# Performance work log

Hardware: AMD Instinct MI355X
Metric: run time of the kernel (lower is better)

Reference implementation:

```python
import jax, jax.numpy as jnp
import numpy as np

B, N, C, K = 32, 1024, 14, 9      # graphs, residues/graph, atom channels, kNN
E, H, NC = 128, 128, 25           # embed_size, hidden_size, num_classes
NG = 128                          # gaussians in time embedding (== embed_size)


def _ffn(x, W1, b1, W2, b2):
    # nn.Sequential(SiLU, Linear, SiLU, Linear)
    h = jax.nn.silu(x) @ W1 + b1
    return jax.nn.silu(h) @ W2 + b2


def _time_emb(t, Wt1, bt1, Wt2, bt2):
    # GaussianSmearing(0,1,NG) -> Linear -> ReLU -> Linear
    offset = jnp.linspace(0.0, 1.0, NG)
    coeff = -0.5 / (offset[1] - offset[0]) ** 2
    d = t[..., None] - offset + 1e-6
    g = jnp.exp(coeff * d * d)
    return jax.nn.relu(g @ Wt1 + bt1) @ Wt2 + bt2


def _forward(S, X, t, emb, Wt1, bt1, Wt2, bt2, We1, be1, We2, be2,
             Wx1, bx1, Wx2, bx2, Wh1, bh1, Wh2, bh2,
             Wd1, bd1, Wd2, bd2, Wp1, bp1, Wr1, br1, Wr2, br2):
    H0 = emb[S]                                           # [B,N,E]
    Hh = H0 + _time_emb(t, Wt1, bt1, Wt2, bt2)            # H_0 + time_emb
    # dynamic kNN graph on CA coordinates (channel 1), per graph
    ca = X[:, :, 1]                                       # [B,N,3]
    d2 = jnp.sum((ca[:, :, None] - ca[:, None]) ** 2, -1) # [B,N,N]
    d2 = d2 + jnp.eye(N, dtype=d2.dtype) * 1e10           # no self loops
    _, idx = jax.lax.top_k(-d2, K)                        # [B,N,K] neighbor ids
    gather = jax.vmap(lambda a, i: a[i])                  # per-graph gather
    Xnb = gather(X, idx)                                  # [B,N,K,C,3]
    Hnb = gather(Hh, idx)                                 # [B,N,K,E]
    rel = X[:, :, None] - Xnb                             # [B,N,K,C,3]
    # multi-channel radial features (EGNN-style channel Gram matrix)
    radial = jnp.einsum('bnkcd,bnked->bnkce', rel, rel).reshape(B, N, K, C * C) / C
    Hi = jnp.broadcast_to(Hh[:, :, None], (B, N, K, E))
    m = _ffn(jnp.concatenate([Hi, Hnb, radial], -1), We1, be1, We2, be2)  # [B,N,K,H]
    # EGNN coordinate update
    w = _ffn(m, Wx1, bx1, Wx2, bx2)                       # [B,N,K,1]
    X_out = X + jnp.mean(rel * w[..., None], axis=2)      # [B,N,C,3]
    # node update
    Hn = Hh + _ffn(jnp.concatenate([Hh, jnp.sum(m, 2)], -1), Wh1, bh1, Wh2, bh2)
    # symmetric edge-distance FFN: f([src,dst]) + f([dst,src])
    Hs = jnp.broadcast_to(Hn[:, :, None], (B, N, K, E))
    Hd = gather(Hn, idx)
    pd = (_ffn(jnp.concatenate([Hs, Hd], -1), Wd1, bd1, Wd2, bd2)
          + _ffn(jnp.concatenate([Hd, Hs], -1), Wd1, bd1, Wd2, bd2))[..., 0]  # [B,N,K]
    # pred_logits = ffn_residue2(pre_H_0 * sigmoid(ffn_proj(H)))
    gate = jax.nn.sigmoid(jax.nn.silu(Hn) @ Wp1 + bp1)
    logits = _ffn(H0 * gate, Wr1, br1, Wr2, br2)          # [B,N,NC]
    return logits, X_out, pd


def setup_inputs() -> dict:
    key = jax.random.key(0)
    ks = jax.random.split(key, 34)
    p = lambda k, s: (0.02 * jax.random.normal(k, s)).astype(jnp.float32)
    inp = {
        'X': jax.random.normal(ks[0], (B, N, C, 3), jnp.float32),
        'S': jax.random.randint(ks[1], (B, N), 0, NC),
        't': jax.random.uniform(ks[2], (B, N), jnp.float32),
        'emb': p(ks[3], (NC, E)),
        'Wt1': p(ks[4], (NG, H)), 'bt1': jnp.zeros((H,), jnp.float32),
        'Wt2': p(ks[5], (H, E)), 'bt2': jnp.zeros((E,), jnp.float32),
        'We1': p(ks[6], (2 * E + C * C, H)), 'be1': jnp.zeros((H,), jnp.float32),
        'We2': p(ks[7], (H, H)), 'be2': jnp.zeros((H,), jnp.float32),
        'Wx1': p(ks[8], (H, H)), 'bx1': jnp.zeros((H,), jnp.float32),
        'Wx2': p(ks[9], (H, 1)), 'bx2': jnp.zeros((1,), jnp.float32),
        'Wh1': p(ks[10], (E + H, H)), 'bh1': jnp.zeros((H,), jnp.float32),
        'Wh2': p(ks[11], (H, E)), 'bh2': jnp.zeros((E,), jnp.float32),
        'Wd1': p(ks[12], (2 * E, H)), 'bd1': jnp.zeros((H,), jnp.float32),
        'Wd2': p(ks[13], (H, 1)), 'bd2': jnp.zeros((1,), jnp.float32),
        'Wp1': p(ks[14], (E, E)), 'bp1': jnp.zeros((E,), jnp.float32),
        'Wr1': p(ks[15], (E, H)), 'br1': jnp.zeros((H,), jnp.float32),
        'Wr2': p(ks[16], (H, NC)), 'br2': jnp.zeros((NC,), jnp.float32),
    }
    return inp


def reference(X, S, t, emb, Wt1, bt1, Wt2, bt2, We1, be1, We2, be2,
              Wx1, bx1, Wx2, bx2, Wh1, bh1, Wh2, bh2,
              Wd1, bd1, Wd2, bd2, Wp1, bp1, Wr1, br1, Wr2, br2):
    return _forward(S, X, t, emb, Wt1, bt1, Wt2, bt2, We1, be1, We2, be2,
                    Wx1, bx1, Wx2, bx2, Wh1, bh1, Wh2, bh2,
                    Wd1, bd1, Wd2, bd2, Wp1, bp1, Wr1, br1, Wr2, br2)
```

## Files before the change

kernel.cpp:

```cpp
#include <hip/hip_runtime.h>

#define BATCH 32
#define NPT   1024
#define CC    14
#define KNN   9
#define EDIM  128
#define HDIM  128
#define NCLS  25
#define BN    (BATCH*NPT)

#define RSTR  132
#define SSTR  140

typedef float  v4f __attribute__((ext_vector_type(4)));
typedef __bf16 v8bf __attribute__((ext_vector_type(8)));

__device__ const unsigned char PC_tab[105] = {
    0,0,0,0,0,0,0,0,0,0,0,0,0,0,
    1,1,1,1,1,1,1,1,1,1,1,1,1,
    2,2,2,2,2,2,2,2,2,2,2,2,
    3,3,3,3,3,3,3,3,3,3,3,
    4,4,4,4,4,4,4,4,4,4,
    5,5,5,5,5,5,5,5,5,
    6,6,6,6,6,6,6,6,
// ... 9 lines not shown
    1,2,3,4,5,6,7,8,9,10,11,12,13,
    2,3,4,5,6,7,8,9,10,11,12,13,
    3,4,5,6,7,8,9,10,11,12,13,
    4,5,6,7,8,9,10,11,12,13,
    5,6,7,8,9,10,11,12,13,
    6,7,8,9,10,11,12,13,
    7,8,9,10,11,12,13,
    8,9,10,11,12,13,
    9,10,11,12,13,
    10,11,12,13,
    11,12,13,
    12,13,
    13};

__device__ __forceinline__ float silu_f(float x) {
    const float e = __expf(-x);
    return x * __builtin_amdgcn_rcpf(1.0f + e);
}
__device__ __forceinline__ float sigm_f(float x) {
    const float e = __expf(-x);
    return __builtin_amdgcn_rcpf(1.0f + e);
}

__device__ __forceinline__ unsigned short f2bf_rne(float f) {
    union { float f; unsigned u; } v; v.f = f;
    unsigned r = v.u + 0x7fffu + ((v.u >> 16) & 1u);
    return (unsigned short)(r >> 16);
}
__device__ __forceinline__ unsigned short f2bf(float f) {
    union { float f; unsigned u; } v; v.f = f;
    return (unsigned short)((v.u + 0x8000u) >> 16);
}

__global__ __launch_bounds__(256) void k_prep(
    const float* __restrict__ We1, const float* __restrict__ We2,
    const float* __restrict__ Wx1, const float* __restrict__ Wh1,
    const float* __restrict__ Wh2, const float* __restrict__ Wd1,
    const float* __restrict__ Wp1, const float* __restrict__ Wr1,
    const float* __restrict__ Wt1, const float* __restrict__ Wt2,
    const float* __restrict__ Wr2,
    unsigned short* __restrict__ WeF,  unsigned short* __restrict__ We2t,
    unsigned short* __restrict__ Wx1t, unsigned short* __restrict__ Wh1t,
    unsigned short* __restrict__ Wh2t, unsigned short* __restrict__ Wd1t,
    unsigned short* __restrict__ Wp1t, unsigned short* __restrict__ Wr1t,
    unsigned short* __restrict__ Wt1t, unsigned short* __restrict__ Wt2t,
    unsigned short* __restrict__ We1Ft, unsigned short* __restrict__ Wr2t)
{
    int i = blockIdx.x * 256 + threadIdx.x;
    if (i < 16384) {
        const int ch = i >> 7, k = i & 127;
        float v = 0.0f;
        if (k < 105) {
            const int c = PC_tab[k], e = PE_tab[k];
            v = We1[(size_t)(256 + c*14 + e)*128 + ch];
            if (c != e) v += We1[(size_t)(256 + e*14 + c)*128 + ch];
        }
        WeF[i] = f2bf_rne(v);
        return;
    }
    i -= 16384;
    if (i < 16384) { We2t[i] = f2bf_rne(We2[(size_t)(i % 128)*128 + i/128]); return; }
    i -= 16384;
    if (i < 16384) { Wx1t[i] = f2bf_rne(Wx1[(size_t)(i % 128)*128 + i/128]); return; }
    i -= 16384;
    if (i < 32768) { const int c = i/256, k = i%256; Wh1t[i] = f2bf_rne(Wh1[(size_t)k*128 + c]); return; }
    i -= 32768;
    if (i < 16384) { Wh2t[i] = f2bf_rne(Wh2[(size_t)(i % 128)*128 + i/128]); return; }
    i -= 16384;
    if (i < 32768) {
        const int t = i/128, k = i%128;
        Wd1t[i] = f2bf_rne((t < 128) ? Wd1[(size_t)k*128 + t] : Wd1[(size_t)(128 + k)*128 + (t - 128)]);
        return;
    }
    i -= 32768;
    if (i < 16384) { Wp1t[i] = f2bf_rne(Wp1[(size_t)(i % 128)*128 + i/128]); return; }
    i -= 16384;
    if (i < 16384) { Wr1t[i] = f2bf_rne(Wr1[(size_t)(i % 128)*128 + i/128]); return; }
    i -= 16384;
    if (i < 16384) { Wt1t[i] = f2bf_rne(Wt1[(size_t)(i % 128)*128 + i/128]); return; }
    i -= 16384;
    if (i < 16384) { Wt2t[i] = f2bf_rne(Wt2[(size_t)(i % 128)*128 + i/128]); return; }
    i -= 16384;
    if (i < 32768) {
        const int t = i/128, k = i%128;
        We1Ft[i] = f2bf_rne((t < 128) ? We1[(size_t)k*128 + t] : We1[(size_t)(128 + k)*128 + (t - 128)]);
        return;
    }
    i -= 32768;
    if (i < 4096) {
        const int ch = i >> 7, k = i & 127;
        Wr2t[i] = (ch < NCLS) ? f2bf_rne(Wr2[(size_t)k*NCLS + ch]) : (unsigned short)0;
    }
}

__global__ __launch_bounds__(256) void k_hhP(
    const float* __restrict__ t, const int* __restrict__ S,
    const float* __restrict__ emb,
    const unsigned short* __restrict__ Wt1t, const float* __restrict__ bt1,
    const unsigned short* __restrict__ Wt2t, const float* __restrict__ bt2,
    const unsigned short* __restrict__ We1Ft, const float* __restrict__ be1,
    float* __restrict__ Hh, float* __restrict__ P)
{
    __shared__ __align__(16) unsigned short A0[32*140];
    __shared__ __align__(16) unsigned short A1[32*140];
    __shared__ __align__(16) unsigned short A2[32*140];
    __shared__ int sInt[32];

    const int tid  = threadIdx.x;
    const int wv   = tid >> 6, lane = tid & 63;
    const int quad = lane >> 4, r16 = lane & 15;
    const int col  = tid & 127, rh = tid >> 7;
    const int base = blockIdx.x * 32;

    if (tid < 32) sInt[tid] = S[base + tid];

    const float step  = 1.0f / 127.0f;
    const float coeff = -0.5f / (step * step);
    const float off   = step * (float)col;
    #pragma unroll
    for (int rr = 0; rr < 16; ++rr) {
        const int r = rh*16 + rr;
        const float d = t[base + r] - off + 1e-6f;
        A0[r*140 + col] = f2bf(__expf(coeff * d * d));
    }
    __syncthreads();

    {
        v8bf a[2][4];
        #pragma unroll
        for (int g = 0; g < 2; ++g)
            #pragma unroll
            for (int ks = 0; ks < 4; ++ks)
                a[g][ks] = *(const v8bf*)(A0 + (16*g + r16)*140 + ks*32 + quad*8);
        #pragma unroll
        for (int c2 = 0; c2 < 2; ++c2) {
            const int ch = (wv*2 + c2)*16 + r16;
            v4f acc[2] = {(v4f){0,0,0,0}, (v4f){0,0,0,0}};
            #pragma unroll
            for (int ks = 0; ks < 4; ++ks) {
                const v8bf bb = *(const v8bf*)(Wt1t + (size_t)ch*128 + ks*32 + quad*8);
                acc[0] = __builtin_amdgcn_mfma_f32_16x16x32_bf16(a[0][ks], bb, acc[0], 0, 0, 0);
                acc[1] = __builtin_amdgcn_mfma_f32_16x16x32_bf16(a[1][ks], bb, acc[1], 0, 0, 0);
            }
            const float bc = bt1[ch];
            #pragma unroll
            for (int g = 0; g < 2; ++g)
                #pragma unroll
                for (int rr = 0; rr < 4; ++rr)
                    A1[(16*g + quad*4 + rr)*140 + ch] = f2bf(fmaxf(acc[g][rr] + bc, 0.0f));
        }
    }
    __syncthreads();

    {
        v8bf a[2][4];
        #pragma unroll
        for (int g = 0; g < 2; ++g)
            #pragma unroll
            for (int ks = 0; ks < 4; ++ks)
                a[g][ks] = *(const v8bf*)(A1 + (16*g + r16)*140 + ks*32 + quad*8);
        #pragma unroll
        for (int c2 = 0; c2 < 2; ++c2) {
            const int ch = (wv*2 + c2)*16 + r16;
            v4f acc[2] = {(v4f){0,0,0,0}, (v4f){0,0,0,0}};
            #pragma unroll
            for (int ks = 0; ks < 4; ++ks) {
                const v8bf bb = *(const v8bf*)(Wt2t + (size_t)ch*128 + ks*32 + quad*8);
                acc[0] = __builtin_amdgcn_mfma_f32_16x16x32_bf16(a[0][ks], bb, acc[0], 0, 0, 0);
                acc[1] = __builtin_amdgcn_mfma_f32_16x16x32_bf16(a[1][ks], bb, acc[1], 0, 0, 0);
            }
            const float bc = bt2[ch];
            #pragma unroll
            for (int g = 0; g < 2; ++g)
                #pragma unroll
                for (int rr = 0; rr < 4; ++rr) {
                    const int row = 16*g + quad*4 + rr;
                    const int node = base + row;
                    const float hh = emb[sInt[row]*128 + ch] + acc[g][rr] + bc;
                    Hh[(size_t)node*128 + ch] = hh;
                    A2[row*140 + ch] = f2bf(silu_f(hh));
                }
        }
    }
    __syncthreads();

    {
        v8bf a[2][4];
        #pragma unroll
        for (int g = 0; g < 2; ++g)
            #pragma unroll
            for (int ks = 0; ks < 4; ++ks)
                a[g][ks] = *(const v8bf*)(A2 + (16*g + r16)*140 + ks*32 + quad*8);
        #pragma unroll
        for (int c2 = 0; c2 < 4; ++c2) {
            const int ch = (wv*4 + c2)*16 + r16;
            v4f acc[2] = {(v4f){0,0,0,0}, (v4f){0,0,0,0}};
            #pragma unroll
            for (int ks = 0; ks < 4; ++ks) {
                const v8bf bb = *(const v8bf*)(We1Ft + (size_t)ch*128 + ks*32 + quad*8);
                acc[0] = __builtin_amdgcn_mfma_f32_16x16x32_bf16(a[0][ks], bb, acc[0], 0, 0, 0);
                acc[1] = __builtin_amdgcn_mfma_f32_16x16x32_bf16(a[1][ks], bb, acc[1], 0, 0, 0);
            }
            const float fb = (ch < 128) ? be1[ch] : 0.0f;
            #pragma unroll
            for (int g = 0; g < 2; ++g)
                #pragma unroll
                for (int rr = 0; rr < 4; ++rr)
                    P[(size_t)(base + 16*g + quad*4 + rr)*256 + ch] = acc[g][rr] + fb;
        }
    }
}

__global__ __launch_bounds__(256) void k_knn(
    const float* __restrict__ X, int* __restrict__ idxb)
{
    __shared__ __align__(16) float4 Cc[NPT];
    __shared__ float dsh[4][64][KNN];
    __shared__ int   ish[4][64][KNN];

    const int tid = threadIdx.x, lane = tid & 63, wv = tid >> 6;
    const int bb = blockIdx.x >> 4;
    const int n0 = (blockIdx.x & 15) << 6;
    const float* Xb = X + (size_t)bb * NPT * 42;

    for (int i = tid; i < NPT; i += 256) {
        const float* p = Xb + (size_t)i*42 + 3;
        Cc[i] = make_float4(p[0], p[1], p[2], 0.0f);
    }
    __syncthreads();

    const int n = n0 + lane;
    const float4 c = Cc[n];

    float dist[KNN]; int ind[KNN];
    #pragma unroll
    for (int k = 0; k < KNN; ++k) { dist[k] = 3.0e38f; ind[k] = -1; }

    const int j0 = wv * 256;
    for (int jj = 0; jj < 256; ++jj) {
        const int j = j0 + jj;
        const float4 q = Cc[j];
        const float dx = __fsub_rn(c.x, q.x);
        const float dy = __fsub_rn(c.y, q.y);
        const float dz = __fsub_rn(c.z, q.z);
        float d = __fadd_rn(__fadd_rn(__fmul_rn(dx,dx), __fmul_rn(dy,dy)), __fmul_rn(dz,dz));
        if (j == n) d = __fadd_rn(d, 1e10f);
        if (d < dist[KNN-1]) {
            dist[KNN-1] = d; ind[KNN-1] = j;
            #pragma unroll
            for (int p = KNN-1; p > 0; --p) {
                if (dist[p] < dist[p-1]) {
                    float td = dist[p]; dist[p] = dist[p-1]; dist[p-1] = td;
                    int   ti = ind[p];  ind[p]  = ind[p-1];  ind[p-1]  = ti;
                }
            }
        }
    }
    #pragma unroll
    for (int k = 0; k < KNN; ++k) { dsh[wv][lane][k] = dist[k]; ish[wv][lane][k] = ind[k]; }
    __syncthreads();

    if (tid < 64) {
        float fd[KNN]; int fi[KNN];
        #pragma unroll
        for (int k = 0; k < KNN; ++k) { fd[k] = 3.0e38f; fi[k] = -1; }
        for (int w = 0; w < 4; ++w)
            #pragma unroll
            for (int k = 0; k < KNN; ++k) {
                const float d = dsh[w][tid][k];
                const int   i = ish[w][tid][k];
                if (d < fd[KNN-1]) {
                    fd[KNN-1] = d; fi[KNN-1] = i;
                    #pragma unroll
                    for (int p = KNN-1; p > 0; --p) {
                        if (fd[p] < fd[p-1]) {
                            float td = fd[p]; fd[p] = fd[p-1]; fd[p-1] = td;
                            int   ti = fi[p]; fi[p] = fi[p-1]; fi[p-1] = ti;
                        }
                    }
                }
            }
        const int node = (bb << 10) + n0 + tid;
        #pragma unroll
        for (int k = 0; k < KNN; ++k) idxb[(size_t)node*KNN + k] = fi[k];
    }
}

__global__ __launch_bounds__(256) void k_edge(
    const float* __restrict__ X, const int* __restrict__ idxb,
    const float* __restrict__ P,
    const unsigned short* __restrict__ WeF,
    const unsigned short* __restrict__ We2t,
    const unsigned short* __restrict__ Wx1t,
    const float* __restrict__ be2,
    const float* __restrict__ bx1, const float* __restrict__ Wx2,
    const float* __restrict__ bx2,
    float* __restrict__ msum, float* __restrict__ wbuf)
{
    __shared__ unsigned short radF[16*RSTR];
    __shared__ unsigned short silA[16*SSTR];
    __shared__ unsigned short silB[16*SSTR];
    __shared__ __align__(16) float relS[16][57];
    __shared__ float wred[KNN][16][4];
    __shared__ int   jsh[16][KNN];

    const int tid  = threadIdx.x;
    const int wv   = tid >> 6, lane = tid & 63;
    const int quad = lane >> 4, r16 = lane & 15;
    const int node0 = blockIdx.x * 16;
    const int b     = node0 >> 10;
    const int chan0 = (wv*2 + 0)*16 + r16;
    const int chan1 = (wv*2 + 1)*16 + r16;
    const int srow  = tid >> 4, c16 = tid & 15;

    if (tid < 144) jsh[tid/9][tid%9] = idxb[(size_t)(node0 + tid/9)*KNN + tid%9];

    int offCE[7];
    #pragma unroll
    for (int kk = 0; kk < 7; ++kk) {
        const int f = c16 + 16*kk;
        if (f < 105) offCE[kk] = ((int)PC_tab[f]*4) | (((int)PE_tab[f]*4) << 16);
        else         offCE[kk] = 0;
    }
    {
        const int f6 = 96 + c16, f7 = 112 + c16;
        if (f6 >= 105) radF[srow*RSTR + f6] = 0;
        radF[srow*RSTR + f7] = 0;
    }

    float xr[3] = {0,0,0};
    if (c16 < 14) {
        #pragma unroll
        for (int k = 0; k < 3; ++k)
            xr[k] = X[(size_t)(node0 + srow)*42 + c16*3 + k];
    }

    float pn0[4], pn1[4];
    #pragma unroll
    for (int rr = 0; rr < 4; ++rr) {
        pn0[rr] = P[(size_t)(node0 + quad*4 + rr)*256 + chan0];
        pn1[rr] = P[(size_t)(node0 + quad*4 + rr)*256 + chan1];
    }
    const float be2c0 = be2[chan0], be2c1 = be2[chan1];
    const float bxc0  = bx1[chan0], bxc1  = bx1[chan1];
    const float wxc0  = Wx2[chan0], wxc1  = Wx2[chan1];

    v8bf B1[2][4], B2[2][4], B3[2][4];
    #pragma unroll
    for (int c2 = 0; c2 < 2; ++c2) {
        const int ct = wv*2 + c2;
        #pragma unroll
        for (int ks = 0; ks < 4; ++ks) {
            B1[c2][ks] = *(const v8bf*)(WeF  + (size_t)(ct*16 + r16)*128 + ks*32 + quad*8);
            B2[c2][ks] = *(const v8bf*)(We2t + (size_t)(ct*16 + r16)*128 + ks*32 + quad*8);
            B3[c2][ks] = *(const v8bf*)(Wx1t + (size_t)(ct*16 + r16)*128 + ks*32 + quad*8);
        }
    }

    float msA0[4] = {0,0,0,0}, msA1[4] = {0,0,0,0};

    __syncthreads();

    float xj[3] = {0,0,0};
    if (c16 < 14) {
        const int j = jsh[srow][0];
        #pragma unroll
        for (int k = 0; k < 3; ++k)
            xj[k] = X[(size_t)((b << 10) + j)*42 + c16*3 + k];
    }

    for (int t = 0; t < KNN; ++t) {
        if (c16 < 14) {
            #pragma unroll
            for (int k = 0; k < 3; ++k)
                relS[srow][c16*4 + k] = xr[k] - xj[k];
        }
        if (t + 1 < KNN && c16 < 14) {
            const int j = jsh[srow][t+1];
            #pragma unroll
            for (int k = 0; k < 3; ++k)
                xj[k] = X[(size_t)((b << 10) + j)*42 + c16*3 + k];
        }
        float pj0[4], pj1[4];
        #pragma unroll
        for (int rr = 0; rr < 4; ++rr) {
            const int jq = jsh[quad*4 + rr][t];
            const size_t jrow = (size_t)((b << 10) + jq)*256 + 128;
            pj0[rr] = P[jrow + chan0];
            pj1[rr] = P[jrow + chan1];
        }

        {
            const float* rb = relS[srow];
            #pragma unroll
            for (int kk = 0; kk < 7; ++kk) {
                const int f = c16 + 16*kk;
                if (f < 105) {
                    const int oc = offCE[kk] & 0xffff, oe = offCE[kk] >> 16;
                    const float v = (rb[oc]*rb[oe] + rb[oc+1]*rb[oe+1]
                                   + rb[oc+2]*rb[oe+2]) * (1.0f/14.0f);
                    radF[srow*RSTR + f] = f2bf(silu_f(v));
                }
            }
        }
        __syncthreads();

        v4f acc10 = (v4f){0,0,0,0}, acc11 = (v4f){0,0,0,0};
        #pragma unroll
        for (int ks = 0; ks < 4; ++ks) {
            const v8bf a = *(const v8bf*)(radF + r16*RSTR + ks*32 + quad*8);
            acc10 = __builtin_amdgcn_mfma_f32_16x16x32_bf16(a, B1[0][ks], acc10, 0, 0, 0);
            acc11 = __builtin_amdgcn_mfma_f32_16x16x32_bf16(a, B1[1][ks], acc11, 0, 0, 0);
        }
        #pragma unroll
        for (int rr = 0; rr < 4; ++rr) {
            const int rw = quad*4 + rr;
            silA[rw*SSTR + chan0] = f2bf(silu_f(acc10[rr] + pn0[rr] + pj0[rr]));
            silA[rw*SSTR + chan1] = f2bf(silu_f(acc11[rr] + pn1[rr] + pj1[rr]));
        }
        __syncthreads();

        v4f acc20 = (v4f){0,0,0,0}, acc21 = (v4f){0,0,0,0};
        #pragma unroll
        for (int ks = 0; ks < 4; ++ks) {
            const v8bf a = *(const v8bf*)(silA + r16*SSTR + ks*32 + quad*8);
            acc20 = __builtin_amdgcn_mfma_f32_16x16x32_bf16(a, B2[0][ks], acc20, 0, 0, 0);
            acc21 = __builtin_amdgcn_mfma_f32_16x16x32_bf16(a, B2[1][ks], acc21, 0, 0, 0);
        }
        #pragma unroll
        for (int rr = 0; rr < 4; ++rr) {
            const float m0 = acc20[rr] + be2c0;
            const float m1 = acc21[rr] + be2c1;
            msA0[rr] += m0;  msA1[rr] += m1;
            const int rw = quad*4 + rr;
            silB[rw*SSTR + chan0] = f2bf(silu_f(m0));
            silB[rw*SSTR + chan1] = f2bf(silu_f(m1));
        }
        __syncthreads();

        v4f acc30 = (v4f){0,0,0,0}, acc31 = (v4f){0,0,0,0};
        #pragma unroll
        for (int ks = 0; ks < 4; ++ks) {
            const v8bf a = *(const v8bf*)(silB + r16*SSTR + ks*32 + quad*8);
            acc30 = __builtin_amdgcn_mfma_f32_16x16x32_bf16(a, B3[0][ks], acc30, 0, 0, 0);
            acc31 = __builtin_amdgcn_mfma_f32_16x16x32_bf16(a, B3[1][ks], acc31, 0, 0, 0);
        }
        #pragma unroll
        for (int rr = 0; rr < 4; ++rr) {
            float pr = silu_f(acc30[rr] + bxc0) * wxc0
                     + silu_f(acc31[rr] + bxc1) * wxc1;
            pr += __shfl_xor(pr, 1);
            pr += __shfl_xor(pr, 2);
            pr += __shfl_xor(pr, 4);
            pr += __shfl_xor(pr, 8);
            if (r16 == 0) wred[t][quad*4 + rr][wv] = pr;
        }
    }

    #pragma unroll
    for (int rr = 0; rr < 4; ++rr) {
        msum[(size_t)(node0 + quad*4 + rr)*128 + chan0] = msA0[rr];
        msum[(size_t)(node0 + quad*4 + rr)*128 + chan1] = msA1[rr];
    }
    __syncthreads();
    if (tid < 16*KNN) {
        const int tt = tid / 16, rw = tid % 16;
        wbuf[(size_t)(node0 + rw)*KNN + tt] =
            wred[tt][rw][0] + wred[tt][rw][1] + wred[tt][rw][2] + wred[tt][rw][3] + bx2[0];
    }
}

__global__ __launch_bounds__(256) void k_nodeF(
    const float* __restrict__ X, const float* __restrict__ Hh,
    const float* __restrict__ msum, const int* __restrict__ idxb,
    const float* __restrict__ wbuf,
    const unsigned short* __restrict__ Wh1t, const float* __restrict__ bh1,
    const unsigned short* __restrict__ Wh2t, const float* __restrict__ bh2,
    const unsigned short* __restrict__ Wd1t, const float* __restrict__ bd1,
    const int* __restrict__ S, const float* __restrict__ emb,
    const unsigned short* __restrict__ Wp1t, const float* __restrict__ bp1,
    const unsigned short* __restrict__ Wr1t, const float* __restrict__ br1,
    const unsigned short* __restrict__ Wr2t, const float* __restrict__ br2,
    float* __restrict__ Hn, float* __restrict__ AB,
    float* __restrict__ outL, float* __restrict__ outX)
{
    __shared__ __align__(16) unsigned short A0[32*268];
    __shared__ __align__(16) unsigned short A1[32*140];
    __shared__ __align__(16) unsigned short A2[32*140];
    __shared__ __align__(16) unsigned short A3[32*140];
    __shared__ int sInt[32];

    const int tid  = threadIdx.x;
    const int wv   = tid >> 6, lane = tid & 63;
    const int quad = lane >> 4, r16 = lane & 15;
    const int base = blockIdx.x * 32;

    if (tid < 32) sInt[tid] = S[base + tid];
    for (int r = 0; r < 32; ++r) {
        const int node = base + r;
        const float v = (tid < 128) ? Hh[(size_t)node*128 + tid]
                                    : msum[(size_t)node*128 + (tid - 128)];
        A0[r*268 + tid] = f2bf(silu_f(v));
    }
    __syncthreads();

    {
        v8bf a[2][8];
        #pragma unroll
        for (int g = 0; g < 2; ++g)
            #pragma unroll
            for (int ks = 0; ks < 8; ++ks)
                a[g][ks] = *(const v8bf*)(A0 + (16*g + r16)*268 + ks*32 + quad*8);
        #pragma unroll
        for (int c2 = 0; c2 < 2; ++c2) {
            const int ch = (wv*2 + c2)*16 + r16;
            v4f acc[2] = {(v4f){0,0,0,0}, (v4f){0,0,0,0}};
            #pragma unroll
            for (int ks = 0; ks < 8; ++ks) {
                const v8bf bb = *(const v8bf*)(Wh1t + (size_t)ch*256 + ks*32 + quad*8);
                acc[0] = __builtin_amdgcn_mfma_f32_16x16x32_bf16(a[0][ks], bb, acc[0], 0, 0, 0);
                acc[1] = __builtin_amdgcn_mfma_f32_16x16x32_bf16(a[1][ks], bb, acc[1], 0, 0, 0);
            }
            const float bc = bh1[ch];
            #pragma unroll
            for (int g = 0; g < 2; ++g)
                #pragma unroll
                for (int rr = 0; rr < 4; ++rr)
                    A1[(16*g + quad*4 + rr)*140 + ch] = f2bf(silu_f(acc[g][rr] + bc));
        }
    }
    __syncthreads();

    {
        v8bf a[2][4];
        #pragma unroll
        for (int g = 0; g < 2; ++g)
            #pragma unroll
            for (int ks = 0; ks < 4; ++ks)
// ... 158 lines not shown

        const float An0 = AB[(size_t)node*256 + c0];
        const float An1 = AB[(size_t)node*256 + c1];
        const float Bn0 = AB[(size_t)node*256 + 128 + c0];
        const float Bn1 = AB[(size_t)node*256 + 128 + c1];

        float Aj0[KNN], Aj1[KNN], Bj0[KNN], Bj1[KNN];
        #pragma unroll
        for (int e = 0; e < KNN; ++e) {
            const size_t jn = (size_t)((b << 10) + __shfl(jv, e)) * 256;
            Aj0[e] = AB[jn + c0];       Aj1[e] = AB[jn + c1];
            Bj0[e] = AB[jn + 128 + c0]; Bj1[e] = AB[jn + 128 + c1];
        }
        #pragma unroll
        for (int e = 0; e < KNN; ++e) {
            float p = (silu_f(An0 + Bj0[e]) + silu_f(Aj0[e] + Bn0)) * w0
                    + (silu_f(An1 + Bj1[e]) + silu_f(Aj1[e] + Bn1)) * w1;
            #pragma unroll
            for (int off = 32; off; off >>= 1) p += __shfl_xor(p, off, 64);
            if (lane == 0) outPd[(size_t)node*KNN + e] = p + b2;
        }
    }
}

extern "C" void kernel_launch(void* const* d_in, const int* in_sizes, int n_in,
                              void* d_out, int out_size, void* d_ws, size_t ws_size,
                              hipStream_t stream)
{
    const float* X   = (const float*)d_in[0];
    const int*   S   = (const int*)  d_in[1];
    const float* t   = (const float*)d_in[2];
    const float* emb = (const float*)d_in[3];
    const float* Wt1 = (const float*)d_in[4];
    const float* bt1 = (const float*)d_in[5];
    const float* Wt2 = (const float*)d_in[6];
    const float* bt2 = (const float*)d_in[7];
    const float* We1 = (const float*)d_in[8];
    const float* be1 = (const float*)d_in[9];
    const float* We2 = (const float*)d_in[10];
    const float* be2 = (const float*)d_in[11];
    const float* Wx1 = (const float*)d_in[12];
    const float* bx1 = (const float*)d_in[13];
    const float* Wx2 = (const float*)d_in[14];
    const float* bx2 = (const float*)d_in[15];
    const float* Wh1 = (const float*)d_in[16];
    const float* bh1 = (const float*)d_in[17];
    const float* Wh2 = (const float*)d_in[18];
    const float* bh2 = (const float*)d_in[19];
    const float* Wd1 = (const float*)d_in[20];
    const float* bd1 = (const float*)d_in[21];
    const float* Wd2 = (const float*)d_in[22];
    const float* bd2 = (const float*)d_in[23];
    const float* Wp1 = (const float*)d_in[24];
    const float* bp1 = (const float*)d_in[25];
    const float* Wr1 = (const float*)d_in[26];
    const float* br1 = (const float*)d_in[27];
    const float* Wr2 = (const float*)d_in[28];
    const float* br2 = (const float*)d_in[29];

    float* out   = (float*)d_out;
    float* outL  = out;
    float* outX  = out + (size_t)BN*NCLS;
    float* outPd = outX + (size_t)BN*CC*3;

    unsigned short* WeF   = (unsigned short*)d_ws;
    unsigned short* We2t  = WeF   + 16384;
    unsigned short* Wx1t  = We2t  + 16384;
    unsigned short* Wh1t  = Wx1t  + 16384;
    unsigned short* Wh2t  = Wh1t  + 32768;
    unsigned short* Wd1t  = Wh2t  + 16384;
    unsigned short* Wp1t  = Wd1t  + 32768;
    unsigned short* Wr1t  = Wp1t  + 16384;
    unsigned short* Wt1t  = Wr1t  + 16384;
    unsigned short* Wt2t  = Wt1t  + 16384;
    unsigned short* We1Ft = Wt2t  + 16384;
    unsigned short* Wr2t  = We1Ft + 32768;
    float* Hh   = (float*)(Wr2t + 4096);
    float* msum = Hh   + (size_t)BN*EDIM;
    float* Hn   = msum + (size_t)BN*HDIM;
    float* wbuf = Hn   + (size_t)BN*EDIM;
    float* P    = wbuf + (size_t)BN*KNN;
    int*   idxb = (int*)(P + (size_t)BN*256);

    k_prep  <<<912,    256, 0, stream>>>(We1, We2, Wx1, Wh1, Wh2, Wd1, Wp1, Wr1, Wt1, Wt2, Wr2,
                                         WeF, We2t, Wx1t, Wh1t, Wh2t, Wd1t, Wp1t, Wr1t,
                                         Wt1t, Wt2t, We1Ft, Wr2t);
    k_hhP   <<<BN/32,  256, 0, stream>>>(t, S, emb, Wt1t, bt1, Wt2t, bt2, We1Ft, be1, Hh, P);
    k_knn   <<<BN/64,  256, 0, stream>>>(X, idxb);
    k_edge  <<<BN/16,  256, 0, stream>>>(X, idxb, P, WeF, We2t, Wx1t,
                                         be2, bx1, Wx2, bx2, msum, wbuf);
    k_nodeF <<<BN/32,  256, 0, stream>>>(X, Hh, msum, idxb, wbuf,
                                         Wh1t, bh1, Wh2t, bh2, Wd1t, bd1,
                                         S, emb, Wp1t, bp1, Wr1t, br1, Wr2t, br2,
                                         Hn, P, outL, outX);
    k_pd2   <<<BN/8,   256, 0, stream>>>(P, idxb, Wd2, bd2, outPd);
}
```

Baseline: 421.8 us.

## Merge time-embedding and kNN kernels; process two neighbor slots per edge iteration

The time-embedding/P projection kernel and the kNN search kernel become one launch, with blocks split by index and sharing a union shared-memory buffer. The two independent workloads can then run concurrently, and one launch is removed. The edge kernel double-buffers its radial, silA and silB tiles so that two neighbor slots share each synchronization phase, and it prefetches the next neighbor's coordinates pre-scaled by 1/sqrt(14). This raises shared-memory and register use per block, which may reduce occupancy.

```diff
diff --git a/kernel.cpp b/kernel.cpp
--- a/kernel.cpp
+++ b/kernel.cpp
@@ -115,8 +115,9 @@
     if (i < 16384) { Wt2t[i] = f2bf_rne(Wt2[(size_t)(i % 128)*128 + i/128]); return; }
     i -= 16384;
     if (i < 32768) {
-        const int t = i/128, k = i%128;
-        We1Ft[i] = f2bf_rne((t < 128) ? We1[(size_t)k*128 + t] : We1[(size_t)(128 + k)*128 + (t - 128)]);
+        const float* q = (i/128 < 128) ? &We1[(size_t)(i%128)*128 + i/128]
+                                       : &We1[(size_t)(128 + i%128)*128 + (i/128 - 128)];
+        We1Ft[i] = f2bf_rne(*q);
         return;
     }
     i -= 32768;
@@ -126,196 +127,204 @@
     }
 }
 
-__global__ __launch_bounds__(256) void k_hhP(
+__global__ __launch_bounds__(256) void k_hhPknn(
     const float* __restrict__ t, const int* __restrict__ S,
     const float* __restrict__ emb,
     const unsigned short* __restrict__ Wt1t, const float* __restrict__ bt1,
     const unsigned short* __restrict__ Wt2t, const float* __restrict__ bt2,
     const unsigned short* __restrict__ We1Ft, const float* __restrict__ be1,
-    float* __restrict__ Hh, float* __restrict__ P)
-{
-    __shared__ __align__(16) unsigned short A0[32*140];
-    __shared__ __align__(16) unsigned short A1[32*140];
-    __shared__ __align__(16) unsigned short A2[32*140];
-    __shared__ int sInt[32];
-
-    const int tid  = threadIdx.x;
-    const int wv   = tid >> 6, lane = tid & 63;
-    const int quad = lane >> 4, r16 = lane & 15;
-    const int col  = tid & 127, rh = tid >> 7;
-    const int base = blockIdx.x * 32;
-
-    if (tid < 32) sInt[tid] = S[base + tid];
-
-    const float step  = 1.0f / 127.0f;
-    const float coeff = -0.5f / (step * step);
-    const float off   = step * (float)col;
-    #pragma unroll
-    for (int rr = 0; rr < 16; ++rr) {
-        const int r = rh*16 + rr;
-        const float d = t[base + r] - off + 1e-6f;
-        A0[r*140 + col] = f2bf(__expf(coeff * d * d));
-    }
-    __syncthreads();
-
-    {
-        v8bf a[2][4];
-        #pragma unroll
-        for (int g = 0; g < 2; ++g)
-            #pragma unroll
-            for (int ks = 0; ks < 4; ++ks)
-                a[g][ks] = *(const v8bf*)(A0 + (16*g + r16)*140 + ks*32 + quad*8);
-        #pragma unroll
-        for (int c2 = 0; c2 < 2; ++c2) {
-            const int ch = (wv*2 + c2)*16 + r16;
-            v4f acc[2] = {(v4f){0,0,0,0}, (v4f){0,0,0,0}};
-            #pragma unroll
-            for (int ks = 0; ks < 4; ++ks) {
-                const v8bf bb = *(const v8bf*)(Wt1t + (size_t)ch*128 + ks*32 + quad*8);
-                acc[0] = __builtin_amdgcn_mfma_f32_16x16x32_bf16(a[0][ks], bb, acc[0], 0, 0, 0);
-                acc[1] = __builtin_amdgcn_mfma_f32_16x16x32_bf16(a[1][ks], bb, acc[1], 0, 0, 0);
-            }
-            const float bc = bt1[ch];
-            #pragma unroll
-            for (int g = 0; g < 2; ++g)
-                #pragma unroll
-                for (int rr = 0; rr < 4; ++rr)
-                    A1[(16*g + quad*4 + rr)*140 + ch] = f2bf(fmaxf(acc[g][rr] + bc, 0.0f));
-        }
-    }
-    __syncthreads();
-
-    {
-        v8bf a[2][4];
-        #pragma unroll
-        for (int g = 0; g < 2; ++g)
-            #pragma unroll
-            for (int ks = 0; ks < 4; ++ks)
-                a[g][ks] = *(const v8bf*)(A1 + (16*g + r16)*140 + ks*32 + quad*8);
-        #pragma unroll
-        for (int c2 = 0; c2 < 2; ++c2) {
-            const int ch = (wv*2 + c2)*16 + r16;
-            v4f acc[2] = {(v4f){0,0,0,0}, (v4f){0,0,0,0}};
-            #pragma unroll
-            for (int ks = 0; ks < 4; ++ks) {
-                const v8bf bb = *(const v8bf*)(Wt2t + (size_t)ch*128 + ks*32 + quad*8);
-                acc[0] = __builtin_amdgcn_mfma_f32_16x16x32_bf16(a[0][ks], bb, acc[0], 0, 0, 0);
-                acc[1] = __builtin_amdgcn_mfma_f32_16x16x32_bf16(a[1][ks], bb, acc[1], 0, 0, 0);
-            }
-            const float bc = bt2[ch];
-            #pragma unroll
-            for (int g = 0; g < 2; ++g)
-                #pragma unroll
-                for (int rr = 0; rr < 4; ++rr) {
-                    const int row = 16*g + quad*4 + rr;
-                    const int node = base + row;
-                    const float hh = emb[sInt[row]*128 + ch] + acc[g][rr] + bc;
-                    Hh[(size_t)node*128 + ch] = hh;
-                    A2[row*140 + ch] = f2bf(silu_f(hh));
-                }
-        }
-    }
-    __syncthreads();
-
-    {
-        v8bf a[2][4];
-        #pragma unroll
-        for (int g = 0; g < 2; ++g)
-            #pragma unroll
-            for (int ks = 0; ks < 4; ++ks)
-                a[g][ks] = *(const v8bf*)(A2 + (16*g + r16)*140 + ks*32 + quad*8);
-        #pragma unroll
-        for (int c2 = 0; c2 < 4; ++c2) {
-            const int ch = (wv*4 + c2)*16 + r16;
-            v4f acc[2] = {(v4f){0,0,0,0}, (v4f){0,0,0,0}};
-            #pragma unroll
-            for (int ks = 0; ks < 4; ++ks) {
-                const v8bf bb = *(const v8bf*)(We1Ft + (size_t)ch*128 + ks*32 + quad*8);
-                acc[0] = __builtin_amdgcn_mfma_f32_16x16x32_bf16(a[0][ks], bb, acc[0], 0, 0, 0);
-                acc[1] = __builtin_amdgcn_mfma_f32_16x16x32_bf16(a[1][ks], bb, acc[1], 0, 0, 0);
-            }
-            const float fb = (ch < 128) ? be1[ch] : 0.0f;
-            #pragma unroll
-            for (int g = 0; g < 2; ++g)
-                #pragma unroll
-                for (int rr = 0; rr < 4; ++rr)
-                    P[(size_t)(base + 16*g + quad*4 + rr)*256 + ch] = acc[g][rr] + fb;
-        }
-    }
-}
-
-__global__ __launch_bounds__(256) void k_knn(
+    float* __restrict__ Hh, float* __restrict__ P,
     const float* __restrict__ X, int* __restrict__ idxb)
 {
-    __shared__ __align__(16) float4 Cc[NPT];
-    __shared__ float dsh[4][64][KNN];
-    __shared__ int   ish[4][64][KNN];
-
-    const int tid = threadIdx.x, lane = tid & 63, wv = tid >> 6;
-    const int bb = blockIdx.x >> 4;
-    const int n0 = (blockIdx.x & 15) << 6;
-    const float* Xb = X + (size_t)bb * NPT * 42;
-
-    for (int i = tid; i < NPT; i += 256) {
-        const float* p = Xb + (size_t)i*42 + 3;
-        Cc[i] = make_float4(p[0], p[1], p[2], 0.0f);
-    }
-    __syncthreads();
-
-    const int n = n0 + lane;
-    const float4 c = Cc[n];
-
-    float dist[KNN]; int ind[KNN];
-    #pragma unroll
-    for (int k = 0; k < KNN; ++k) { dist[k] = 3.0e38f; ind[k] = -1; }
-
-    const int j0 = wv * 256;
-    for (int jj = 0; jj < 256; ++jj) {
-        const int j = j0 + jj;
-        const float4 q = Cc[j];
-        const float dx = __fsub_rn(c.x, q.x);
-        const float dy = __fsub_rn(c.y, q.y);
-        const float dz = __fsub_rn(c.z, q.z);
-        float d = __fadd_rn(__fadd_rn(__fmul_rn(dx,dx), __fmul_rn(dy,dy)), __fmul_rn(dz,dz));
-        if (j == n) d = __fadd_rn(d, 1e10f);
-        if (d < dist[KNN-1]) {
-            dist[KNN-1] = d; ind[KNN-1] = j;
-            #pragma unroll
-            for (int p = KNN-1; p > 0; --p) {
-                if (dist[p] < dist[p-1]) {
-                    float td = dist[p]; dist[p] = dist[p-1]; dist[p-1] = td;
-                    int   ti = ind[p];  ind[p]  = ind[p-1];  ind[p-1]  = ti;
-                }
-            }
-        }
-    }
-    #pragma unroll
-    for (int k = 0; k < KNN; ++k) { dsh[wv][lane][k] = dist[k]; ish[wv][lane][k] = ind[k]; }
-    __syncthreads();
-
-    if (tid < 64) {
-        float fd[KNN]; int fi[KNN];
-        #pragma unroll
-        for (int k = 0; k < KNN; ++k) { fd[k] = 3.0e38f; fi[k] = -1; }
-        for (int w = 0; w < 4; ++w)
-            #pragma unroll
-            for (int k = 0; k < KNN; ++k) {
-                const float d = dsh[w][tid][k];
-                const int   i = ish[w][tid][k];
-                if (d < fd[KNN-1]) {
-                    fd[KNN-1] = d; fi[KNN-1] = i;
+    __shared__ __align__(16) unsigned char smem[34816];
+    const int tid = threadIdx.x;
+
+    if (blockIdx.x < BN/32) {
+        unsigned short* A0 = (unsigned short*)smem;
+        unsigned short* A1 = A0 + 32*140;
+        unsigned short* A2 = A1 + 32*140;
+        int*            sInt = (int*)(A2 + 32*140);
+
+        const int wv   = tid >> 6, lane = tid & 63;
+        const int quad = lane >> 4, r16 = lane & 15;
+        const int col  = tid & 127, rh = tid >> 7;
+        const int base = blockIdx.x * 32;
+
+        if (tid < 32) sInt[tid] = S[base + tid];
+
+        const float step  = 1.0f / 127.0f;
+        const float coeff = -0.5f / (step * step);
+        const float off   = step * (float)col;
+        #pragma unroll
+        for (int rr = 0; rr < 16; ++rr) {
+            const int r = rh*16 + rr;
+            const float d = t[base + r] - off + 1e-6f;
+            A0[r*140 + col] = f2bf(__expf(coeff * d * d));
+        }
+        __syncthreads();
+
+        {
+            v8bf a[2][4];
+            #pragma unroll
+            for (int g = 0; g < 2; ++g)
+                #pragma unroll
+                for (int ks = 0; ks < 4; ++ks)
+                    a[g][ks] = *(const v8bf*)(A0 + (16*g + r16)*140 + ks*32 + quad*8);
+            #pragma unroll
+            for (int c2 = 0; c2 < 2; ++c2) {
+                const int ch = (wv*2 + c2)*16 + r16;
+                v4f acc[2] = {(v4f){0,0,0,0}, (v4f){0,0,0,0}};
+                #pragma unroll
+                for (int ks = 0; ks < 4; ++ks) {
+                    const v8bf bb = *(const v8bf*)(Wt1t + (size_t)ch*128 + ks*32 + quad*8);
+                    acc[0] = __builtin_amdgcn_mfma_f32_16x16x32_bf16(a[0][ks], bb, acc[0], 0, 0, 0);
+                    acc[1] = __builtin_amdgcn_mfma_f32_16x16x32_bf16(a[1][ks], bb, acc[1], 0, 0, 0);
+                }
+                const float bc = bt1[ch];
+                #pragma unroll
+                for (int g = 0; g < 2; ++g)
                     #pragma unroll
-                    for (int p = KNN-1; p > 0; --p) {
-                        if (fd[p] < fd[p-1]) {
-                            float td = fd[p]; fd[p] = fd[p-1]; fd[p-1] = td;
-                            int   ti = fi[p]; fi[p] = fi[p-1]; fi[p-1] = ti;
+                    for (int rr = 0; rr < 4; ++rr)
+                        A1[(16*g + quad*4 + rr)*140 + ch] = f2bf(fmaxf(acc[g][rr] + bc, 0.0f));
+            }
+        }
+        __syncthreads();
+
+        {
+            v8bf a[2][4];
+            #pragma unroll
+            for (int g = 0; g < 2; ++g)
+                #pragma unroll
+                for (int ks = 0; ks < 4; ++ks)
+                    a[g][ks] = *(const v8bf*)(A1 + (16*g + r16)*140 + ks*32 + quad*8);
+            #pragma unroll
+            for (int c2 = 0; c2 < 2; ++c2) {
+                const int ch = (wv*2 + c2)*16 + r16;
+                v4f acc[2] = {(v4f){0,0,0,0}, (v4f){0,0,0,0}};
+                #pragma unroll
+                for (int ks = 0; ks < 4; ++ks) {
+                    const v8bf bb = *(const v8bf*)(Wt2t + (size_t)ch*128 + ks*32 + quad*8);
+                    acc[0] = __builtin_amdgcn_mfma_f32_16x16x32_bf16(a[0][ks], bb, acc[0], 0, 0, 0);
+                    acc[1] = __builtin_amdgcn_mfma_f32_16x16x32_bf16(a[1][ks], bb, acc[1], 0, 0, 0);
+                }
+                const float bc = bt2[ch];
+                #pragma unroll
+                for (int g = 0; g < 2; ++g)
+                    #pragma unroll
+                    for (int rr = 0; rr < 4; ++rr) {
+                        const int row = 16*g + quad*4 + rr;
+                        const int node = base + row;
+                        const float hh = emb[sInt[row]*128 + ch] + acc[g][rr] + bc;
+                        Hh[(size_t)node*128 + ch] = hh;
+                        A2[row*140 + ch] = f2bf(silu_f(hh));
+                    }
+            }
+        }
+        __syncthreads();
+
+        {
+            v8bf a[2][4];
+            #pragma unroll
+            for (int g = 0; g < 2; ++g)
+                #pragma unroll
+                for (int ks = 0; ks < 4; ++ks)
+                    a[g][ks] = *(const v8bf*)(A2 + (16*g + r16)*140 + ks*32 + quad*8);
+            #pragma unroll
+            for (int c2 = 0; c2 < 4; ++c2) {
+                const int ch = (wv*4 + c2)*16 + r16;
+                v4f acc[2] = {(v4f){0,0,0,0}, (v4f){0,0,0,0}};
+                #pragma unroll
+                for (int ks = 0; ks < 4; ++ks) {
+                    const v8bf bb = *(const v8bf*)(We1Ft + (size_t)ch*128 + ks*32 + quad*8);
+                    acc[0] = __builtin_amdgcn_mfma_f32_16x16x32_bf16(a[0][ks], bb, acc[0], 0, 0, 0);
+                    acc[1] = __builtin_amdgcn_mfma_f32_16x16x32_bf16(a[1][ks], bb, acc[1], 0, 0, 0);
+                }
+                const float fb = (ch < 128) ? be1[ch] : 0.0f;
+                #pragma unroll
+                for (int g = 0; g < 2; ++g)
+                    #pragma unroll
+                    for (int rr = 0; rr < 4; ++rr)
+                        P[(size_t)(base + 16*g + quad*4 + rr)*256 + ch] = acc[g][rr] + fb;
+            }
+        }
+        return;
+    }
+
+    {
+        float4* Cc   = (float4*)smem;
+        float*  dshp = (float*)(smem + 16384);
+        int*    ishp = (int*)  (smem + 25600);
+
+        const int kb = blockIdx.x - BN/32;
+        const int lane = tid & 63, wv = tid >> 6;
+        const int bb = kb >> 4;
+        const int n0 = (kb & 15) << 6;
+        const float* Xb = X + (size_t)bb * NPT * 42;
+
+        for (int i = tid; i < NPT; i += 256) {
+            const float* p = Xb + (size_t)i*42 + 3;
+            Cc[i] = make_float4(p[0], p[1], p[2], 0.0f);
+        }
+        __syncthreads();
+
+        const int n = n0 + lane;
+        const float4 c = Cc[n];
+
+        float dist[KNN]; int ind[KNN];
+        #pragma unroll
+        for (int k = 0; k < KNN; ++k) { dist[k] = 3.0e38f; ind[k] = -1; }
+
+        const int j0 = wv * 256;
+        for (int jj = 0; jj < 256; ++jj) {
+            const int j = j0 + jj;
+            const float4 q = Cc[j];
+            const float dx = __fsub_rn(c.x, q.x);
+            const float dy = __fsub_rn(c.y, q.y);
+            const float dz = __fsub_rn(c.z, q.z);
+            float d = __fadd_rn(__fadd_rn(__fmul_rn(dx,dx), __fmul_rn(dy,dy)), __fmul_rn(dz,dz));
+            if (j == n) d = __fadd_rn(d, 1e10f);
+            if (d < dist[KNN-1]) {
+                dist[KNN-1] = d; ind[KNN-1] = j;
+                #pragma unroll
+                for (int p = KNN-1; p > 0; --p) {
+                    if (dist[p] < dist[p-1]) {
+                        float td = dist[p]; dist[p] = dist[p-1]; dist[p-1] = td;
+                        int   ti = ind[p];  ind[p]  = ind[p-1];  ind[p-1]  = ti;
+                    }
+                }
+            }
+        }
+        #pragma unroll
+        for (int k = 0; k < KNN; ++k) {
+            dshp[((wv*64 + lane))*KNN + k] = dist[k];
+            ishp[((wv*64 + lane))*KNN + k] = ind[k];
+        }
+        __syncthreads();
+
+        if (tid < 64) {
+            float fd[KNN]; int fi[KNN];
+            #pragma unroll
+            for (int k = 0; k < KNN; ++k) { fd[k] = 3.0e38f; fi[k] = -1; }
+            for (int w = 0; w < 4; ++w)
+                #pragma unroll
+                for (int k = 0; k < KNN; ++k) {
+                    const float d = dshp[(w*64 + tid)*KNN + k];
+                    const int   i = ishp[(w*64 + tid)*KNN + k];
+                    if (d < fd[KNN-1]) {
+                        fd[KNN-1] = d; fi[KNN-1] = i;
+                        #pragma unroll
+                        for (int p = KNN-1; p > 0; --p) {
+                            if (fd[p] < fd[p-1]) {
+                                float td = fd[p]; fd[p] = fd[p-1]; fd[p-1] = td;
+                                int   ti = fi[p]; fi[p] = fi[p-1]; fi[p-1] = ti;
+                            }
                         }
                     }
                 }
-            }
-        const int node = (bb << 10) + n0 + tid;
-        #pragma unroll
-        for (int k = 0; k < KNN; ++k) idxb[(size_t)node*KNN + k] = fi[k];
+            const int node = (bb << 10) + n0 + tid;
+            #pragma unroll
+            for (int k = 0; k < KNN; ++k) idxb[(size_t)node*KNN + k] = fi[k];
+        }
     }
 }
 
@@ -330,9 +339,9 @@
     const float* __restrict__ bx2,
     float* __restrict__ msum, float* __restrict__ wbuf)
 {
-    __shared__ unsigned short radF[16*RSTR];
-    __shared__ unsigned short silA[16*SSTR];
-    __shared__ unsigned short silB[16*SSTR];
+    __shared__ unsigned short radF[2][16*RSTR];
+    __shared__ unsigned short silA[2][16*SSTR];
+    __shared__ unsigned short silB[2][16*SSTR];
     __shared__ __align__(16) float relS[16][57];
     __shared__ float wred[KNN][16][4];
     __shared__ int   jsh[16][KNN];
@@ -345,6 +354,7 @@
     const int chan0 = (wv*2 + 0)*16 + r16;
     const int chan1 = (wv*2 + 1)*16 + r16;
     const int srow  = tid >> 4, c16 = tid & 15;
+    const float s14 = 0.26726124f;
 
     if (tid < 144) jsh[tid/9][tid%9] = idxb[(size_t)(node0 + tid/9)*KNN + tid%9];
 
@@ -357,15 +367,18 @@
     }
     {
         const int f6 = 96 + c16, f7 = 112 + c16;
-        if (f6 >= 105) radF[srow*RSTR + f6] = 0;
-        radF[srow*RSTR + f7] = 0;
+        #pragma unroll
+        for (int s = 0; s < 2; ++s) {
+            if (f6 >= 105) radF[s][srow*RSTR + f6] = 0;
+            radF[s][srow*RSTR + f7] = 0;
+        }
     }
 
     float xr[3] = {0,0,0};
     if (c16 < 14) {
         #pragma unroll
         for (int k = 0; k < 3; ++k)
-            xr[k] = X[(size_t)(node0 + srow)*42 + c16*3 + k];
+            xr[k] = X[(size_t)(node0 + srow)*42 + c16*3 + k] * s14;
     }
 
     float pn0[4], pn1[4];
@@ -394,99 +407,123 @@
 
     __syncthreads();
 
-    float xj[3] = {0,0,0};
+    float xj[2][3] = {{0,0,0},{0,0,0}};
     if (c16 < 14) {
-        const int j = jsh[srow][0];
-        #pragma unroll
-        for (int k = 0; k < 3; ++k)
-            xj[k] = X[(size_t)((b << 10) + j)*42 + c16*3 + k];
-    }
-
-    for (int t = 0; t < KNN; ++t) {
-        if (c16 < 14) {
+        #pragma unroll
+        for (int s = 0; s < 2; ++s) {
+            const int j = jsh[srow][s];
             #pragma unroll
             for (int k = 0; k < 3; ++k)
-                relS[srow][c16*4 + k] = xr[k] - xj[k];
-        }
-        if (t + 1 < KNN && c16 < 14) {
-            const int j = jsh[srow][t+1];
-            #pragma unroll
-            for (int k = 0; k < 3; ++k)
-                xj[k] = X[(size_t)((b << 10) + j)*42 + c16*3 + k];
-        }
-        float pj0[4], pj1[4];
-        #pragma unroll
-        for (int rr = 0; rr < 4; ++rr) {
-            const int jq = jsh[quad*4 + rr][t];
-            const size_t jrow = (size_t)((b << 10) + jq)*256 + 128;
-            pj0[rr] = P[jrow + chan0];
-            pj1[rr] = P[jrow + chan1];
-        }
-
-        {
-            const float* rb = relS[srow];
-            #pragma unroll
-            for (int kk = 0; kk < 7; ++kk) {
-                const int f = c16 + 16*kk;
-                if (f < 105) {
-                    const int oc = offCE[kk] & 0xffff, oe = offCE[kk] >> 16;
-                    const float v = (rb[oc]*rb[oe] + rb[oc+1]*rb[oe+1]
-                                   + rb[oc+2]*rb[oe+2]) * (1.0f/14.0f);
-                    radF[srow*RSTR + f] = f2bf(silu_f(v));
-                }
-            }
-        }
+                xj[s][k] = X[(size_t)((b << 10) + j)*42 + c16*3 + k] * s14;
+        }
+    }
+
+    for (int tp = 0; tp < KNN; tp += 2) {
+        const int ns = (tp + 1 < KNN) ? 2 : 1;
+
+        #pragma unroll
+        for (int s = 0; s < 2; ++s) {
+            if (s < ns) {
+                if (c16 < 14) {
+                    #pragma unroll
+                    for (int k = 0; k < 3; ++k)
+                        relS[srow][c16*4 + k] = xr[k] - xj[s][k];
+                }
+                if (tp + 2 + s < KNN && c16 < 14) {
+                    const int j = jsh[srow][tp + 2 + s];
+                    #pragma unroll
+                    for (int k = 0; k < 3; ++k)
+                        xj[s][k] = X[(size_t)((b << 10) + j)*42 + c16*3 + k] * s14;
+                }
+                const float* rb = relS[srow];
+                #pragma unroll
+                for (int kk = 0; kk < 7; ++kk) {
+                    const int f = c16 + 16*kk;
+                    if (f < 105) {
+                        const int oc = offCE[kk] & 0xffff, oe = offCE[kk] >> 16;
+                        const float v = rb[oc]*rb[oe] + rb[oc+1]*rb[oe+1] + rb[oc+2]*rb[oe+2];
+                        radF[s][srow*RSTR + f] = f2bf(silu_f(v));
+                    }
+                }
+            }
+        }
+        float pj0[2][4], pj1[2][4];
+        #pragma unroll
+        for (int s = 0; s < 2; ++s)
+            if (s < ns)
+                #pragma unroll
+                for (int rr = 0; rr < 4; ++rr) {
+                    const int jq = jsh[quad*4 + rr][tp + s];
+                    const size_t jrow = (size_t)((b << 10) + jq)*256 + 128;
+                    pj0[s][rr] = P[jrow + chan0];
+                    pj1[s][rr] = P[jrow + chan1];
+                }
         __syncthreads();
 
-        v4f acc10 = (v4f){0,0,0,0}, acc11 = (v4f){0,0,0,0};
-        #pragma unroll
-        for (int ks = 0; ks < 4; ++ks) {
-            const v8bf a = *(const v8bf*)(radF + r16*RSTR + ks*32 + quad*8);
-            acc10 = __builtin_amdgcn_mfma_f32_16x16x32_bf16(a, B1[0][ks], acc10, 0, 0, 0);
-            acc11 = __builtin_amdgcn_mfma_f32_16x16x32_bf16(a, B1[1][ks], acc11, 0, 0, 0);
-        }
-        #pragma unroll
-        for (int rr = 0; rr < 4; ++rr) {
-            const int rw = quad*4 + rr;
-            silA[rw*SSTR + chan0] = f2bf(silu_f(acc10[rr] + pn0[rr] + pj0[rr]));
-            silA[rw*SSTR + chan1] = f2bf(silu_f(acc11[rr] + pn1[rr] + pj1[rr]));
+        #pragma unroll
+        for (int s = 0; s < 2; ++s) {
+            if (s < ns) {
+                v4f a0 = (v4f){0,0,0,0}, a1 = (v4f){0,0,0,0};
+                #pragma unroll
+                for (int ks = 0; ks < 4; ++ks) {
+                    const v8bf a = *(const v8bf*)(radF[s] + r16*RSTR + ks*32 + quad*8);
+                    a0 = __builtin_amdgcn_mfma_f32_16x16x32_bf16(a, B1[0][ks], a0, 0, 0, 0);
+                    a1 = __builtin_amdgcn_mfma_f32_16x16x32_bf16(a, B1[1][ks], a1, 0, 0, 0);
+                }
+                #pragma unroll
+                for (int rr = 0; rr < 4; ++rr) {
+                    const int rw = quad*4 + rr;
+                    silA[s][rw*SSTR + chan0] = f2bf(silu_f(a0[rr] + pn0[rr] + pj0[s][rr]));
+                    silA[s][rw*SSTR + chan1] = f2bf(silu_f(a1[rr] + pn1[rr] + pj1[s][rr]));
+                }
+            }
         }
         __syncthreads();
 
-        v4f acc20 = (v4f){0,0,0,0}, acc21 = (v4f){0,0,0,0};
-        #pragma unroll
-        for (int ks = 0; ks < 4; ++ks) {
-            const v8bf a = *(const v8bf*)(silA + r16*SSTR + ks*32 + quad*8);
-            acc20 = __builtin_amdgcn_mfma_f32_16x16x32_bf16(a, B2[0][ks], acc20, 0, 0, 0);
-            acc21 = __builtin_amdgcn_mfma_f32_16x16x32_bf16(a, B2[1][ks], acc21, 0, 0, 0);
-        }
-        #pragma unroll
-        for (int rr = 0; rr < 4; ++rr) {
-            const float m0 = acc20[rr] + be2c0;
-            const float m1 = acc21[rr] + be2c1;
-            msA0[rr] += m0;  msA1[rr] += m1;
-            const int rw = quad*4 + rr;
-            silB[rw*SSTR + chan0] = f2bf(silu_f(m0));
-            silB[rw*SSTR + chan1] = f2bf(silu_f(m1));
+        #pragma unroll
+        for (int s = 0; s < 2; ++s) {
+            if (s < ns) {
+                v4f a0 = (v4f){0,0,0,0}, a1 = (v4f){0,0,0,0};
+                #pragma unroll
+                for (int ks = 0; ks < 4; ++ks) {
+                    const v8bf a = *(const v8bf*)(silA[s] + r16*SSTR + ks*32 + quad*8);
+                    a0 = __builtin_amdgcn_mfma_f32_16x16x32_bf16(a, B2[0][ks], a0, 0, 0, 0);
+                    a1 = __builtin_amdgcn_mfma_f32_16x16x32_bf16(a, B2[1][ks], a1, 0, 0, 0);
+                }
+                #pragma unroll
+                for (int rr = 0; rr < 4; ++rr) {
+                    const float m0 = a0[rr] + be2c0;
+                    const float m1 = a1[rr] + be2c1;
+                    msA0[rr] += m0;  msA1[rr] += m1;
+                    const int rw = quad*4 + rr;
+                    silB[s][rw*SSTR + chan0] = f2bf(silu_f(m0));
+                    silB[s][rw*SSTR + chan1] = f2bf(silu_f(m1));
+                }
+            }
         }
         __syncthreads();
 
-        v4f acc30 = (v4f){0,0,0,0}, acc31 = (v4f){0,0,0,0};
-        #pragma unroll
-        for (int ks = 0; ks < 4; ++ks) {
-            const v8bf a = *(const v8bf*)(silB + r16*SSTR + ks*32 + quad*8);
-            acc30 = __builtin_amdgcn_mfma_f32_16x16x32_bf16(a, B3[0][ks], acc30, 0, 0, 0);
-            acc31 = __builtin_amdgcn_mfma_f32_16x16x32_bf16(a, B3[1][ks], acc31, 0, 0, 0);
-        }
-        #pragma unroll
-        for (int rr = 0; rr < 4; ++rr) {
-            float pr = silu_f(acc30[rr] + bxc0) * wxc0
-                     + silu_f(acc31[rr] + bxc1) * wxc1;
-            pr += __shfl_xor(pr, 1);
-            pr += __shfl_xor(pr, 2);
-            pr += __shfl_xor(pr, 4);
-            pr += __shfl_xor(pr, 8);
-            if (r16 == 0) wred[t][quad*4 + rr][wv] = pr;
+        #pragma unroll
+        for (int s = 0; s < 2; ++s) {
+            if (s < ns) {
+                v4f a0 = (v4f){0,0,0,0}, a1 = (v4f){0,0,0,0};
+                #pragma unroll
+                for (int ks = 0; ks < 4; ++ks) {
+                    const v8bf a = *(const v8bf*)(silB[s] + r16*SSTR + ks*32 + quad*8);
+                    a0 = __builtin_amdgcn_mfma_f32_16x16x32_bf16(a, B3[0][ks], a0, 0, 0, 0);
+                    a1 = __builtin_amdgcn_mfma_f32_16x16x32_bf16(a, B3[1][ks], a1, 0, 0, 0);
+                }
+                #pragma unroll
+                for (int rr = 0; rr < 4; ++rr) {
+                    float pr = silu_f(a0[rr] + bxc0) * wxc0
+                             + silu_f(a1[rr] + bxc1) * wxc1;
+                    pr += __shfl_xor(pr, 1);
+                    pr += __shfl_xor(pr, 2);
+                    pr += __shfl_xor(pr, 4);
+                    pr += __shfl_xor(pr, 8);
+                    if (r16 == 0) wred[tp + s][quad*4 + rr][wv] = pr;
+                }
+            }
         }
     }
 
@@ -811,16 +848,16 @@
     float* P    = wbuf + (size_t)BN*KNN;
     int*   idxb = (int*)(P + (size_t)BN*256);
 
-    k_prep  <<<912,    256, 0, stream>>>(We1, We2, Wx1, Wh1, Wh2, Wd1, Wp1, Wr1, Wt1, Wt2, Wr2,
-                                         WeF, We2t, Wx1t, Wh1t, Wh2t, Wd1t, Wp1t, Wr1t,
-                                         Wt1t, Wt2t, We1Ft, Wr2t);
-    k_hhP   <<<BN/32,  256, 0, stream>>>(t, S, emb, Wt1t, bt1, Wt2t, bt2, We1Ft, be1, Hh, P);
-    k_knn   <<<BN/64,  256, 0, stream>>>(X, idxb);
-    k_edge  <<<BN/16,  256, 0, stream>>>(X, idxb, P, WeF, We2t, Wx1t,
-                                         be2, bx1, Wx2, bx2, msum, wbuf);
-    k_nodeF <<<BN/32,  256, 0, stream>>>(X, Hh, msum, idxb, wbuf,
-                                         Wh1t, bh1, Wh2t, bh2, Wd1t, bd1,
-                                         S, emb, Wp1t, bp1, Wr1t, br1, Wr2t, br2,
-                                         Hn, P, outL, outX);
-    k_pd2   <<<BN/8,   256, 0, stream>>>(P, idxb, Wd2, bd2, outPd);
-}
+    k_prep   <<<912,            256, 0, stream>>>(We1, We2, Wx1, Wh1, Wh2, Wd1, Wp1, Wr1, Wt1, Wt2, Wr2,
+                                                  WeF, We2t, Wx1t, Wh1t, Wh2t, Wd1t, Wp1t, Wr1t,
+                                                  Wt1t, Wt2t, We1Ft, Wr2t);
+    k_hhPknn <<<BN/32 + BN/64,  256, 0, stream>>>(t, S, emb, Wt1t, bt1, Wt2t, bt2, We1Ft, be1,
+                                                  Hh, P, X, idxb);
+    k_edge   <<<BN/16,          256, 0, stream>>>(X, idxb, P, WeF, We2t, Wx1t,
+                                                  be2, bx1, Wx2, bx2, msum, wbuf);
+    k_nodeF  <<<BN/32,          256, 0, stream>>>(X, Hh, msum, idxb, wbuf,
+                                                  Wh1t, bh1, Wh2t, bh2, Wd1t, bd1,
+                                                  S, emb, Wp1t, bp1, Wr1t, br1, Wr2t, br2,
+                                                  Hn, P, outL, outX);
+    k_pd2    <<<BN/8,           256, 0, stream>>>(P, idxb, Wd2, bd2, outPd);
+}
```

Measured after the change: 423.5 us. Within noise of the previous version (+0.4%).
